# Performance work log

Measured on AMD Instinct MI355X. Metric: run time of the kernel, lower is better.

The kernel has to match this reference:

```python
import jax, jax.numpy as jnp
import numpy as np

M, K, N = 131072, 512, 512


def setup_inputs() -> dict:
    key = jax.random.key(0)
    k1, k2, k3, k4 = jax.random.split(key, 4)
    # Simulated int8 quantized values held in float32 (real kernel uses int8)
    x = jnp.round(jax.random.normal(k1, (M, K), dtype=jnp.float32) * 30.0)
    weight = jnp.round(jax.random.normal(k2, (N, K), dtype=jnp.float32) * 30.0)
    # per-token activation scale [M,1], per-output-channel weight scale [N]
    x_scale = jax.random.uniform(k3, (M, 1), dtype=jnp.float32, minval=1e-3, maxval=2e-2)
    weight_scale = jax.random.uniform(k4, (N,), dtype=jnp.float32, minval=1e-3, maxval=2e-2)
    return {"x": x, "x_scale": x_scale, "weight": weight, "weight_scale": weight_scale}


def reference(x, x_scale, weight, weight_scale):
    # gemm_a8w8(per_Token): out[m,n] = (sum_k x[m,k]*W[n,k]) * x_scale[m] * w_scale[n]
    acc = jnp.einsum('mk,nk->mn', x, weight)          # [M, N] int32-equivalent accum
    out = acc * x_scale * weight_scale[None, :]       # fused dequant scaling
    return out  # otype would be bf16 in the original; kept fp32 as reference baseline
```

## Files before the change

### kernel.cpp

```cpp
#include <hip/hip_runtime.h>
#include <hip/hip_bf16.h>
#include <stdint.h>

#define K_DIM 512
#define N_DIM 512
#define BM 64
#define PHASE_K 128
#define PHASE_FLOATS (BM * PHASE_K)

typedef __bf16 bf16x8 __attribute__((ext_vector_type(8)));
typedef float floatx4 __attribute__((ext_vector_type(4)));

__device__ __forceinline__ bf16x8 cvt8(float4 a, float4 b) {
    bf16x8 r;
    r[0] = (__bf16)a.x; r[1] = (__bf16)a.y; r[2] = (__bf16)a.z; r[3] = (__bf16)a.w;
    r[4] = (__bf16)b.x; r[5] = (__bf16)b.y; r[6] = (__bf16)b.z; r[7] = (__bf16)b.w;
    return r;
}

__global__ __launch_bounds__(512) void wconv_kernel(const float* __restrict__ w,
                                                    __bf16* __restrict__ wf) {
    int t = blockIdx.x * 512 + threadIdx.x;
    int lane = t & 63, slot = t >> 6;
    int n = ((slot >> 4) << 4) + (lane & 15);
    int k = ((slot & 15) << 5) + ((lane >> 4) << 3);
    const float* src = w + (size_t)n * K_DIM + k;
    float4 f0 = *(const float4*)src;
    float4 f1 = *(const float4*)(src + 4);
    *(bf16x8*)(wf + (size_t)t * 8) = cvt8(f0, f1);
}

__device__ __forceinline__ void stage_phase(const float* __restrict__ x,
                                            int rowBase, int kBase,
                                            float* ldsBuf, int wid, int lane) {
    #pragma unroll
    for (int i = 0; i < 4; ++i) {
        int sl = i * 8 + wid;
        int row = sl * 2 + (lane >> 5);
        int srcByte = ((lane & 31) * 16) ^ ((row & 7) << 4);
        const float* g = x + (size_t)(rowBase + row) * K_DIM + kBase + (srcByte >> 2);
        float* l = ldsBuf + sl * 256;
        __builtin_amdgcn_global_load_lds(
            (const __attribute__((address_space(1))) void*)g,
            (__attribute__((address_space(3))) void*)l, 16, 0, 0);
    }
}

__device__ __forceinline__ bf16x8 read_afrag(const float* ldsBuf, int rt, int kcl, int lane) {
    int row = rt * 16 + (lane & 15);
    int sw = (row & 7) << 4;
    int b0 = kcl * 128 + ((lane >> 4) << 5);
    const char* rb = (const char*)(ldsBuf + row * PHASE_K);
    float4 fa = *(const float4*)(rb + (b0 ^ sw));
    float4 fb = *(const float4*)(rb + ((b0 + 16) ^ sw));
    return cvt8(fa, fb);
}

template <bool USE_WF>
__global__ __launch_bounds__(512, 4) void gemm_kernel(
    const float* __restrict__ x, const float* __restrict__ xscale,
    const __bf16* __restrict__ wf, const float* __restrict__ w,
    const float* __restrict__ wscale, float* __restrict__ out)
{
    __shared__ __align__(16) float lds[2 * PHASE_FLOATS];
    const int t = threadIdx.x;
    const int lane = t & 63;
    const int wid = t >> 6;
    const int laneR = lane & 15;
    const int colb = wid * 64;
    const int rowb = blockIdx.x * BM;

    floatx4 acc[4][4];
    #pragma unroll
    for (int i = 0; i < 4; ++i)
        #pragma unroll
        for (int j = 0; j < 4; ++j) acc[i][j] = (floatx4)0.f;

    stage_phase(x, rowb, 0, lds, wid, lane);

    #pragma unroll
    for (int p = 0; p < 4; ++p) {
        __syncthreads();

        if (p < 3)
            stage_phase(x, rowb, (p + 1) * PHASE_K, &lds[((p + 1) & 1) * PHASE_FLOATS],
                        wid, lane);

        const float* cb = &lds[(p & 1) * PHASE_FLOATS];
        #pragma unroll
        for (int kcl = 0; kcl < 4; ++kcl) {
            const int kcg = p * 4 + kcl;
            bf16x8 ax[4];
            #pragma unroll
            for (int rt = 0; rt < 4; ++rt)
                ax[rt] = read_afrag(cb, rt, kcl, lane);
            #pragma unroll
            for (int nt = 0; nt < 4; ++nt) {
                bf16x8 bw;
                if (USE_WF) {
                    int ntg = (wid << 2) + nt;
                    bw = *(const bf16x8*)(wf + (size_t)(((ntg << 4) + kcg) * 64 + lane) * 8);
                } else {
                    int n = colb + (nt << 4) + laneR;
                    const float* src = w + (size_t)n * K_DIM + (kcg << 5) + ((lane >> 4) << 3);
                    bw = cvt8(*(const float4*)src, *(const float4*)(src + 4));
                }
                #pragma unroll
                for (int rt = 0; rt < 4; ++rt)
                    acc[rt][nt] = __builtin_amdgcn_mfma_f32_16x16x32_bf16(
                        bw, ax[rt], acc[rt][nt], 0, 0, 0);
            }
        }
    }

    #pragma unroll
    for (int rt = 0; rt < 4; ++rt) {
        int m = rowb + rt * 16 + laneR;
        float xs = xscale[m];
        #pragma unroll
        for (int nt = 0; nt < 4; ++nt) {
            int nb = colb + (nt << 4) + ((lane >> 4) << 2);
            float4 wsc = *(const float4*)(wscale + nb);
            floatx4 a = acc[rt][nt];
            float4 o;
            o.x = a[0] * xs * wsc.x;
            o.y = a[1] * xs * wsc.y;
            o.z = a[2] * xs * wsc.z;
            o.w = a[3] * xs * wsc.w;
            *(float4*)(out + (size_t)m * N_DIM + nb) = o;
        }
    }
}

extern "C" void kernel_launch(void* const* d_in, const int* in_sizes, int n_in,
                              void* d_out, int out_size, void* d_ws, size_t ws_size,
                              hipStream_t stream) {
    const float* x      = (const float*)d_in[0];
    const float* xscale = (const float*)d_in[1];
    const float* w      = (const float*)d_in[2];
    const float* wscale = (const float*)d_in[3];
    float* out          = (float*)d_out;

    const int M = in_sizes[0] / K_DIM;
    const int grid = M / BM;

    if (ws_size >= (size_t)(N_DIM * K_DIM * sizeof(unsigned short))) {
        __bf16* wfp = (__bf16*)d_ws;
        wconv_kernel<<<dim3(64), dim3(512), 0, stream>>>(w, wfp);
        gemm_kernel<true><<<dim3(grid), dim3(512), 0, stream>>>(
            x, xscale, wfp, w, wscale, out);
    } else {
        gemm_kernel<false><<<dim3(grid), dim3(512), 0, stream>>>(
            x, xscale, nullptr, w, wscale, out);
    }
}
```

Measured before the change: 198.4 us.

## Split N across two blocks with triple-buffered LDS and manual waitcnt pipeline

Each block now computes a 64x256 half of the output tile, and its 8 waves are arranged as 2 row groups by 4 column groups, so grid size doubles and per-wave accumulators halve. The K phase shrinks to 64, with three LDS buffers. Weight fragments are preloaded into registers per phase. The single __syncthreads is replaced by an explicit s_waitcnt vmcnt(2)/s_barrier sequence with sched_barriers so the next global_load_lds stays in flight during compute. Each X tile is now read from global memory by two blocks, which doubles activation traffic on a memory-bound problem; the gains are meant to come from more occupancy and overlap.

```diff
diff --git a/kernel.cpp b/kernel.cpp
--- a/kernel.cpp
+++ b/kernel.cpp
@@ -5,8 +5,10 @@
 #define K_DIM 512
 #define N_DIM 512
 #define BM 64
-#define PHASE_K 128
+#define BN 256
+#define PHASE_K 64
 #define PHASE_FLOATS (BM * PHASE_K)
+#define NBUF 3
 
 typedef __bf16 bf16x8 __attribute__((ext_vector_type(8)));
 typedef float floatx4 __attribute__((ext_vector_type(4)));
@@ -34,10 +36,10 @@
                                             int rowBase, int kBase,
                                             float* ldsBuf, int wid, int lane) {
     #pragma unroll
-    for (int i = 0; i < 4; ++i) {
+    for (int i = 0; i < 2; ++i) {
         int sl = i * 8 + wid;
-        int row = sl * 2 + (lane >> 5);
-        int srcByte = ((lane & 31) * 16) ^ ((row & 7) << 4);
+        int row = sl * 4 + (lane >> 4);
+        int srcByte = ((lane & 15) << 4) ^ ((row & 7) << 4);
         const float* g = x + (size_t)(rowBase + row) * K_DIM + kBase + (srcByte >> 2);
         float* l = ldsBuf + sl * 256;
         __builtin_amdgcn_global_load_lds(
@@ -46,8 +48,9 @@
     }
 }
 
-__device__ __forceinline__ bf16x8 read_afrag(const float* ldsBuf, int rt, int kcl, int lane) {
-    int row = rt * 16 + (lane & 15);
+__device__ __forceinline__ bf16x8 read_afrag(const float* ldsBuf, int mg, int rt,
+                                             int kcl, int lane) {
+    int row = mg * 32 + rt * 16 + (lane & 15);
     int sw = (row & 7) << 4;
     int b0 = kcl * 128 + ((lane >> 4) << 5);
     const char* rb = (const char*)(ldsBuf + row * PHASE_K);
@@ -57,69 +60,95 @@
 }
 
 template <bool USE_WF>
+__device__ __forceinline__ void load_wfrag(bf16x8 (&dst)[4][2], int p,
+                                           const __bf16* __restrict__ wf,
+                                           const float* __restrict__ w,
+                                           int ntgBase, int lane) {
+    #pragma unroll
+    for (int nt = 0; nt < 4; ++nt) {
+        int ntg = ntgBase + nt;
+        #pragma unroll
+        for (int kcl = 0; kcl < 2; ++kcl) {
+            int kcg = p * 2 + kcl;
+            if (USE_WF) {
+                dst[nt][kcl] = *(const bf16x8*)(wf + (size_t)(((ntg << 4) + kcg) * 64 + lane) * 8);
+            } else {
+                int n = (ntg << 4) + (lane & 15);
+                const float* s = w + (size_t)n * K_DIM + (kcg << 5) + ((lane >> 4) << 3);
+                dst[nt][kcl] = cvt8(*(const float4*)s, *(const float4*)(s + 4));
+            }
+        }
+    }
+}
+
+template <bool USE_WF>
 __global__ __launch_bounds__(512, 4) void gemm_kernel(
     const float* __restrict__ x, const float* __restrict__ xscale,
     const __bf16* __restrict__ wf, const float* __restrict__ w,
     const float* __restrict__ wscale, float* __restrict__ out)
 {
-    __shared__ __align__(16) float lds[2 * PHASE_FLOATS];
+    __shared__ __align__(16) float lds[NBUF * PHASE_FLOATS];
     const int t = threadIdx.x;
     const int lane = t & 63;
     const int wid = t >> 6;
+    const int mg = wid >> 2;
+    const int ng = wid & 3;
     const int laneR = lane & 15;
-    const int colb = wid * 64;
-    const int rowb = blockIdx.x * BM;
 
-    floatx4 acc[4][4];
+    const int bid = blockIdx.x;
+    const int tile = bid >> 1;
+    const int half = bid & 1;
+    const int rowb = tile * BM;
+    const int ntgBase = half * 16 + ng * 4;
+
+    floatx4 acc[2][4];
     #pragma unroll
-    for (int i = 0; i < 4; ++i)
+    for (int i = 0; i < 2; ++i)
         #pragma unroll
         for (int j = 0; j < 4; ++j) acc[i][j] = (floatx4)0.f;
 
+    bf16x8 wfr[4][2];
+
     stage_phase(x, rowb, 0, lds, wid, lane);
+    __builtin_amdgcn_sched_barrier(0);
 
     #pragma unroll
-    for (int p = 0; p < 4; ++p) {
-        __syncthreads();
+    for (int p = 0; p < 8; ++p) {
+        load_wfrag<USE_WF>(wfr, p, wf, w, ntgBase, lane);
+        __builtin_amdgcn_sched_barrier(0);
 
-        if (p < 3)
-            stage_phase(x, rowb, (p + 1) * PHASE_K, &lds[((p + 1) & 1) * PHASE_FLOATS],
-                        wid, lane);
+        if (p < 7) {
+            stage_phase(x, rowb, (p + 1) * PHASE_K,
+                        lds + ((p + 1) % NBUF) * PHASE_FLOATS, wid, lane);
+            __builtin_amdgcn_sched_barrier(0);
+            asm volatile("s_waitcnt vmcnt(2) lgkmcnt(0)\n\ts_barrier" ::: "memory");
+        } else {
+            asm volatile("s_waitcnt vmcnt(0) lgkmcnt(0)\n\ts_barrier" ::: "memory");
+        }
 
-        const float* cb = &lds[(p & 1) * PHASE_FLOATS];
+        const float* cb = lds + (p % NBUF) * PHASE_FLOATS;
         #pragma unroll
-        for (int kcl = 0; kcl < 4; ++kcl) {
-            const int kcg = p * 4 + kcl;
-            bf16x8 ax[4];
+        for (int kcl = 0; kcl < 2; ++kcl) {
+            bf16x8 ax[2];
             #pragma unroll
-            for (int rt = 0; rt < 4; ++rt)
-                ax[rt] = read_afrag(cb, rt, kcl, lane);
+            for (int rt = 0; rt < 2; ++rt)
+                ax[rt] = read_afrag(cb, mg, rt, kcl, lane);
             #pragma unroll
-            for (int nt = 0; nt < 4; ++nt) {
-                bf16x8 bw;
-                if (USE_WF) {
-                    int ntg = (wid << 2) + nt;
-                    bw = *(const bf16x8*)(wf + (size_t)(((ntg << 4) + kcg) * 64 + lane) * 8);
-                } else {
-                    int n = colb + (nt << 4) + laneR;
-                    const float* src = w + (size_t)n * K_DIM + (kcg << 5) + ((lane >> 4) << 3);
-                    bw = cvt8(*(const float4*)src, *(const float4*)(src + 4));
-                }
+            for (int nt = 0; nt < 4; ++nt)
                 #pragma unroll
-                for (int rt = 0; rt < 4; ++rt)
+                for (int rt = 0; rt < 2; ++rt)
                     acc[rt][nt] = __builtin_amdgcn_mfma_f32_16x16x32_bf16(
-                        bw, ax[rt], acc[rt][nt], 0, 0, 0);
-            }
+                        wfr[nt][kcl], ax[rt], acc[rt][nt], 0, 0, 0);
         }
     }
 
     #pragma unroll
-    for (int rt = 0; rt < 4; ++rt) {
-        int m = rowb + rt * 16 + laneR;
+    for (int rt = 0; rt < 2; ++rt) {
+        int m = rowb + mg * 32 + rt * 16 + laneR;
         float xs = xscale[m];
         #pragma unroll
         for (int nt = 0; nt < 4; ++nt) {
-            int nb = colb + (nt << 4) + ((lane >> 4) << 2);
+            int nb = half * BN + ng * 64 + (nt << 4) + ((lane >> 4) << 2);
             float4 wsc = *(const float4*)(wscale + nb);
             floatx4 a = acc[rt][nt];
             float4 o;
@@ -142,7 +171,7 @@
     float* out          = (float*)d_out;
 
     const int M = in_sizes[0] / K_DIM;
-    const int grid = M / BM;
+    const int grid = (M / BM) * 2;
 
     if (ws_size >= (size_t)(N_DIM * K_DIM * sizeof(unsigned short))) {
         __bf16* wfp = (__bf16*)d_ws;
```

After: 217.8 us. 1.1x slower.
